# Kernel optimization log

Hardware: AMD Instinct MI355X
Metric: run time of the kernel (lower is better)

Reference implementation:

```python
import jax, jax.numpy as jnp
import numpy as np

B, T, D, K = 64, 4096, 90, 32
LOG2PI = 1.8378770664093453


def setup_inputs() -> dict:
    key = jax.random.key(0)
    k1, k2, k3, k4, k5 = jax.random.split(key, 5)
    X = jax.random.normal(k1, (B, T, D), dtype=jnp.float32)
    state_priors = jax.random.uniform(k2, (K,), dtype=jnp.float32)
    transition_matrix = jax.random.uniform(k3, (K, K), dtype=jnp.float32)
    mu = jax.random.normal(k4, (K, D), dtype=jnp.float32) * 0.5
    log_var = jax.random.normal(k5, (K, D), dtype=jnp.float32) * 0.1
    return {"X": X, "state_priors": state_priors,
            "transition_matrix": transition_matrix, "mu": mu, "log_var": log_var}


def _emission_logprobs(X, mu, log_var):
    # Diagonal-Gaussian log density per state: (B,T,K)
    # expand (x-mu)^2*inv_var to avoid materializing a (B,T,K,D) tensor
    inv_var = jnp.exp(-log_var)                                   # (K,D)
    quad = (jnp.einsum('btd,kd->btk', X * X, inv_var)
            - 2.0 * jnp.einsum('btd,kd->btk', X, mu * inv_var)
            + jnp.sum(mu * mu * inv_var, axis=-1))                # (B,T,K)
    return -0.5 * (quad + jnp.sum(log_var, axis=-1) + D * LOG2PI)


def reference(X, state_priors, transition_matrix, mu, log_var):
    log_A = jax.nn.log_softmax(transition_matrix, axis=1)   # (K,K)
    log_pi = jax.nn.log_softmax(state_priors, axis=0)       # (K,)
    em = _emission_logprobs(X, mu, log_var)                 # (B,T,K)

    log_alpha0 = log_pi + em[:, 0, :]                       # (B,K)

    def step(log_alpha, e_t):
        # log_alpha: (B,K), e_t: (B,K)
        la = e_t + jax.nn.logsumexp(log_alpha[:, :, None] + log_A[None], axis=1)
        return la, None

    em_rest = jnp.swapaxes(em[:, 1:, :], 0, 1)              # (T-1,B,K)
    log_alpha_T, _ = jax.lax.scan(step, log_alpha0, em_rest)
    # sum over subjects of logsumexp over states at final timestep
    return jnp.sum(jax.nn.logsumexp(log_alpha_T, axis=-1))
```

## Files before the change

### kernel.cpp

```cpp
#include <hip/hip_runtime.h>
#include <stdint.h>

#define B_ 64
#define T_ 4096
#define D_ 90
#define K_ 32
#define CH_ 32
#define F_  128
#define NB_ 2048

typedef float f32x16 __attribute__((ext_vector_type(16)));
typedef __bf16 bf16x8 __attribute__((ext_vector_type(8)));

#define WS_A     0
#define WS_PI    1024
#define WS_C0    1056
#define WS_WF    1088
#define WS_EACC  4160
#define WS_MS    12352
#define WS_E0    20544
#define WS_Q2    22080

#define LDS_XOFF(w) ((w) * 768)
#define LDS_WF      3072
#define LDS_TOT     9216

__device__ __forceinline__ int perm_r(int r) {
  int t2 = (r >> 2) & 3;
  return r + ((t2 == 1) ? 4 : (t2 == 2) ? -4 : 0);
}
__device__ __forceinline__ uint32_t pk2(float hi, float lo) {
  return __builtin_amdgcn_perm(__float_as_uint(hi), __float_as_uint(lo), 0x07060302u);
}
__device__ __forceinline__ uint32_t rnd_pk(float hi, float lo) {
  uint32_t uh = __float_as_uint(hi) + 0x8000u;
  uint32_t ul = __float_as_uint(lo) + 0x8000u;
  return __builtin_amdgcn_perm(uh, ul, 0x07060302u);
}
__device__ __forceinline__ float bf2f(ushort u) {
  return __uint_as_float(((uint32_t)u) << 16);
}
__device__ __forceinline__ bf16x8 mkbf(uint32_t a, uint32_t b, uint32_t c, uint32_t d) {
  union { uint32_t u[4]; bf16x8 v; } x;
  x.u[0] = a; x.u[1] = b; x.u[2] = c; x.u[3] = d;
  return x.v;
}

__global__ __launch_bounds__(1024) void prep_kernel(
    const float* __restrict__ priors, const float* __restrict__ trans,
    const float* __restrict__ mu, const float* __restrict__ lv,
    float* __restrict__ ws) {
  int tid = threadIdx.x;
  {
    float v = trans[tid];
    float m = v;
    #pragma unroll
    for (int mk = 16; mk; mk >>= 1) m = fmaxf(m, __shfl_xor(m, mk));
    float e = expf(v - m);
    float s = e;
    #pragma unroll
    for (int mk = 16; mk; mk >>= 1) s += __shfl_xor(s, mk);
    ws[WS_A + tid] = e / s;
  }
  if (tid < 32) {
    float v = priors[tid];
    float m = v;
    #pragma unroll
    for (int mk = 16; mk; mk >>= 1) m = fmaxf(m, __shfl_xor(m, mk));
    float e = expf(v - m);
    float s = e;
    #pragma unroll
    for (int mk = 16; mk; mk >>= 1) s += __shfl_xor(s, mk);
    ws[WS_PI + tid] = e / s;
  }
  for (int i = tid; i < 6144; i += 1024) {
    int j = i & 7, l = (i >> 3) & 63, cm = i >> 9;
    int c = cm >> 1, mat = cm & 1;
    int h = l >> 5, nn = l & 31;
    int d = 16 * c + 8 * h + j;
    float v = 0.0f;
    if (d < D_) {
      float ivd = expf(-lv[nn * D_ + d]);
      v = (mat == 0) ? -0.5f * ivd : mu[nn * D_ + d] * ivd;
    }
    ((ushort*)(ws + WS_WF))[i] = (ushort)((__float_as_uint(v) + 0x8000u) >> 16);
  }
  if (tid < 32) {
    float s = 0.0f;
    for (int d = 0; d < D_; ++d) {
      float l  = lv[tid * D_ + d];
      float iv = expf(-l);
      float m_ = mu[tid * D_ + d];
      s += m_ * m_ * iv + l;
    }
    ws[WS_C0 + tid] = -0.5f * (s + (float)D_ * 1.8378770664093453f);
  }
}

__global__ __launch_bounds__(256, 8) void fused_kernel(const float* __restrict__ X,
                                                       float* __restrict__ ws,
                                                       float* __restrict__ out) {
  __shared__ __align__(16) ushort sh[LDS_TOT];
  __shared__ float msb[4];
  __shared__ int   peb[4];
  int tid = threadIdx.x;
  int l = tid & 63, w = tid >> 6;
  int n = l & 31, h = l >> 5;
  int tB = blockIdx.x << 7;
  int t0 = tB + (w << 5);
  int b  = t0 >> 12;
  if (blockIdx.x == 0 && tid == 0) *out = 0.0f;

  {
    const uint4* wfp = (const uint4*)((const ushort*)(ws + WS_WF));
    uint4* wfl = (uint4*)(sh + LDS_WF);
    #pragma unroll
    for (int k = 0; k < 3; ++k) wfl[tid + (k << 8)] = wfp[tid + (k << 8)];
  }
  float c0 = ws[WS_C0 + n];

  int srow = l >> 1, sp = l & 1;
  const float* xg = X + (size_t)(t0 + srow) * D_ + 8 * sp;
  ushort* xbuf = sh + LDS_XOFF(w);
  float2 va[4];
  auto xload = [&](int c) {
    #pragma unroll
    for (int s = 0; s < 4; ++s) {
      int d = 16 * c + 8 * sp + 2 * s;
      if (d < D_) va[s] = *(const float2*)(xg + 16 * c + 2 * s);
      else { va[s].x = 0.0f; va[s].y = 0.0f; }
    }
  };
  auto xwrite = [&]() {
    uint4 pkv;
    pkv.x = rnd_pk(va[0].y, va[0].x);
    pkv.y = rnd_pk(va[1].y, va[1].x);
    pkv.z = rnd_pk(va[2].y, va[2].x);
    pkv.w = rnd_pk(va[3].y, va[3].x);
    *(uint4*)(xbuf + srow * 24 + 8 * sp) = pkv;
  };
  xload(0);
  xwrite();
  xload(1);
  __syncthreads();

  const ushort* wfl = sh + LDS_WF;
  f32x16 acc;
  #pragma unroll
  for (int r = 0; r < 16; ++r) acc[r] = 0.0f;
  #pragma unroll
  for (int c = 0; c < 6; ++c) {
    union { uint4 u; bf16x8 v; } xb;
    xb.u = *(const uint4*)(xbuf + n * 24 + 8 * h);
    float x[8];
    #pragma unroll
    for (int j = 0; j < 8; ++j) {
      uint32_t uu = ((const uint32_t*)&xb.u)[j >> 1];
      x[j] = bf2f((j & 1) ? (ushort)(uu >> 16) : (ushort)(uu & 0xFFFF));
    }
    union { uint32_t u[4]; bf16x8 v; } x2b;
    #pragma unroll
    for (int r = 0; r < 4; ++r)
      x2b.u[r] = rnd_pk(x[2*r+1] * x[2*r+1], x[2*r] * x[2*r]);
    union { uint4 u; bf16x8 v; } w1, w2;
    w2.u = *(const uint4*)(wfl + (2 * c)     * 512 + l * 8);
    w1.u = *(const uint4*)(wfl + (2 * c + 1) * 512 + l * 8);
    acc = __builtin_amdgcn_mfma_f32_32x32x16_bf16(xb.v,  w1.v, acc, 0, 0, 0);
    acc = __builtin_amdgcn_mfma_f32_32x32x16_bf16(x2b.v, w2.v, acc, 0, 0, 0);
    if (c < 5) {
      xwrite();
      if (c < 4) xload(c + 2);
    }
  }
  float em[16], mrow[16];
  #pragma unroll
  for (int r = 0; r < 16; ++r) {
    float v = acc[r] + c0;
    em[r] = v;
    float m = v;
    #pragma unroll
    for (int mk = 1; mk <= 16; mk <<= 1) m = fmaxf(m, __shfl_xor(m, mk));
    mrow[r] = m;
  }
  uint32_t ebf[8];
  #pragma unroll
  for (int q = 0; q < 4; ++q) {
    float e0 = exp2f((em[4*q]   - mrow[4*q])   * 1.44269504088896f);
    float e1 = exp2f((em[4*q+1] - mrow[4*q+1]) * 1.44269504088896f);
    float e2 = exp2f((em[4*q+2] - mrow[4*q+2]) * 1.44269504088896f);
    float e3 = exp2f((em[4*q+3] - mrow[4*q+3]) * 1.44269504088896f);
    ebf[2*q]     = rnd_pk(e1, e0);
    ebf[2*q + 1] = rnd_pk(e3, e2);
  }
  bool first = ((t0 & (T_ - 1)) == 0);
  if (first && h == 0)
    ((ushort*)(ws + WS_E0))[b * K_ + n] = (ushort)(ebf[0] & 0xFFFF);
  float msum = 0.0f;
  #pragma unroll
  for (int r = 0; r < 16; ++r) msum += mrow[r];
  msum += __shfl_xor(msum, 32);
  if (l == 0) msb[w] = msum;
  __syncthreads();

  int col = perm_r(n);
  const float* A = ws + WS_A;
  float astat[16];
  #pragma unroll
  for (int j = 0; j < 8; ++j) {
    astat[j]     = A[(8 * h + j) * K_ + col];
    astat[8 + j] = A[(16 + 8 * h + j) * K_ + col];
  }
  uint32_t q[8];
  #pragma unroll
  for (int r = 0; r < 4; ++r) {
    int s0 = 8 * h + 2 * r;
    uint32_t lo = (s0 == n)     ? 0x3F80u : 0u;
    uint32_t hi = (s0 + 1 == n) ? 0x3F80u : 0u;
    q[r] = lo | (hi << 16);
    int s2 = s0 + 16;
    lo = (s2 == n)     ? 0x3F80u : 0u;
    hi = (s2 + 1 == n) ? 0x3F80u : 0u;
    q[4 + r] = lo | (hi << 16);
  }
  int eacc = 0;
  const f32x16 z = {0.f,0.f,0.f,0.f,0.f,0.f,0.f,0.f,0.f,0.f,0.f,0.f,0.f,0.f,0.f,0.f};
  #pragma unroll
  for (int r = 0; r < 16; ++r) acc[r] = 0.0f;

  auto step = [&](float e0) {
    uint32_t au[8];
    #pragma unroll
    for (int r = 0; r < 4; ++r) {
      au[r]     = pk2(astat[2 * r + 1] * e0, astat[2 * r] * e0);
      au[4 + r] = pk2(astat[8 + 2 * r + 1] * e0, astat[8 + 2 * r] * e0);
    }
    bf16x8 alo = mkbf(au[0], au[1], au[2], au[3]);
    bf16x8 ahi = mkbf(au[4], au[5], au[6], au[7]);
    bf16x8 qlo = mkbf(q[0], q[1], q[2], q[3]);
    bf16x8 qhi = mkbf(q[4], q[5], q[6], q[7]);
    acc = __builtin_amdgcn_mfma_f32_32x32x16_bf16(alo, qlo, z, 0, 0, 0);
    acc = __builtin_amdgcn_mfma_f32_32x32x16_bf16(ahi, qhi, acc, 0, 0, 0);
    #pragma unroll
    for (int r = 0; r < 4; ++r) {
      q[r]     = pk2(acc[2 * r + 1], acc[2 * r]);
      q[4 + r] = pk2(acc[8 + 2 * r + 1], acc[8 + 2 * r]);
    }
  };
  auto lmul = [&](uint4 lo, uint4 hi) {
    bf16x8 alo = mkbf(lo.x, lo.y, lo.z, lo.w);
    bf16x8 ahi = mkbf(hi.x, hi.y, hi.z, hi.w);
    bf16x8 qlo = mkbf(q[0], q[1], q[2], q[3]);
    bf16x8 qhi = mkbf(q[4], q[5], q[6], q[7]);
    acc = __builtin_amdgcn_mfma_f32_32x32x16_bf16(alo, qlo, z, 0, 0, 0);
    acc = __builtin_amdgcn_mfma_f32_32x32x16_bf16(ahi, qhi, acc, 0, 0, 0);
    #pragma unroll
    for (int r = 0; r < 4; ++r) {
      q[r]     = pk2(acc[2 * r + 1], acc[2 * r]);
      q[4 + r] = pk2(acc[8 + 2 * r + 1], acc[8 + 2 * r]);
    }
  };
  auto renorm = [&]() {
    float m = acc[0];
    #pragma unroll
    for (int r = 1; r < 16; ++r) m = fmaxf(m, acc[r]);
    #pragma unroll
    for (int mk = 1; mk <= 32; mk <<= 1) m = fmaxf(m, __shfl_xor(m, mk));
    int ex;
    frexpf(m, &ex);
    float sc = ldexpf(1.0f, -ex);
    eacc += ex;
    #pragma unroll
    for (int r = 0; r < 16; ++r) acc[r] *= sc;
    #pragma unroll
    for (int r = 0; r < 4; ++r) {
      q[r]     = pk2(acc[2 * r + 1], acc[2 * r]);
      q[4 + r] = pk2(acc[8 + 2 * r + 1], acc[8 + 2 * r]);
    }
  };

  int src0 = col, src1 = col + 32;
  #pragma unroll
  for (int t = 0; t < 32; ++t) {
    uint32_t ed = (uint32_t)__shfl((int)ebf[2 * (t >> 3) + ((t >> 1) & 1)],
                                   ((t >> 2) & 1) ? src1 : src0);
    float e0 = bf2f((t & 1) ? (ushort)(ed >> 16) : (ushort)(ed & 0xFFFF));
    if (t > 0) step(e0);
    else if (!first) step(e0);
    if ((t & 7) == 7) renorm();
  }

  ushort* Qw = sh + w * 1280;
  #pragma unroll
  for (int r = 0; r < 16; ++r) {
    int m_ = (r & 3) + 8 * (r >> 2) + 4 * h;
    Qw[perm_r(m_) * 40 + n] = (ushort)(__float_as_uint(acc[r]) >> 16);
  }
  if (l == 0) peb[w] = eacc;
  __syncthreads();
  if (w != 0) return;

  #pragma unroll
  for (int r = 0; r < 4; ++r) {
    int s0 = 8 * h + 2 * r;
    uint32_t lo = (s0 == n)     ? 0x3F80u : 0u;
    uint32_t hi = (s0 + 1 == n) ? 0x3F80u : 0u;
    q[r] = lo | (hi << 16);
    int s2 = s0 + 16;
    lo = (s2 == n)     ? 0x3F80u : 0u;
    hi = (s2 + 1 == n) ? 0x3F80u : 0u;
    q[4 + r] = lo | (hi << 16);
  }
  eacc = peb[0] + peb[1] + peb[2] + peb[3];
  float msm = msb[0] + msb[1] + msb[2] + msb[3];
  #pragma unroll
  for (int p = 0; p < 4; ++p) {
    const ushort* base = sh + p * 1280 + col * 40;
    uint4 lo = *(const uint4*)(base + 8 * h);
    uint4 hi = *(const uint4*)(base + 16 + 8 * h);
    lmul(lo, hi);
  }
  renorm();
  ushort* Qo = (ushort*)(ws + WS_Q2) + (size_t)blockIdx.x * (K_ * K_);
  #pragma unroll
  for (int r = 0; r < 16; ++r) {
    int m_ = (r & 3) + 8 * (r >> 2) + 4 * h;
    Qo[perm_r(m_) * K_ + n] = (ushort)(__float_as_uint(acc[r]) >> 16);
  }
  if (l == 0) {
    ((int*)ws)[WS_EACC + blockIdx.x] = eacc;
    ws[WS_MS + blockIdx.x] = msm;
  }
}

__global__ __launch_bounds__(256) void combine_kernel(float* __restrict__ ws,
                                                      float* __restrict__ out) {
  __shared__ __align__(16) ushort pm[4][1280];
  __shared__ int pe[4];
  int tid = threadIdx.x;
  int l = tid & 63, w = tid >> 6;
  int h = l >> 5, n = l & 31;
  int b = blockIdx.x;
  int row = perm_r(n);
  int eacc;
  {
    const int* ea = ((const int*)ws) + WS_EACC + b * 32 + w * 8;
    int v = (l < 8) ? ea[l] : 0;
    #pragma unroll
    for (int mk = 1; mk <= 4; mk <<= 1) v += __shfl_xor(v, mk);
    eacc = __shfl(v, 0);
  }
  uint32_t q[8];
  #pragma unroll
  for (int r = 0; r < 4; ++r) {
    int s0 = 8 * h + 2 * r;
    uint32_t lo = (s0 == n)     ? 0x3F80u : 0u;
    uint32_t hi = (s0 + 1 == n) ? 0x3F80u : 0u;
    q[r] = lo | (hi << 16);
    int s2 = s0 + 16;
    lo = (s2 == n)     ? 0x3F80u : 0u;
    hi = (s2 + 1 == n) ? 0x3F80u : 0u;
    q[4 + r] = lo | (hi << 16);
  }
  f32x16 acc;
  #pragma unroll
  for (int r = 0; r < 16; ++r) acc[r] = 0.0f;
  const f32x16 z = {0.f,0.f,0.f,0.f,0.f,0.f,0.f,0.f,0.f,0.f,0.f,0.f,0.f,0.f,0.f,0.f};

  auto lmul = [&](uint4 lo, uint4 hi) {
    bf16x8 alo = mkbf(lo.x, lo.y, lo.z, lo.w);
    bf16x8 ahi = mkbf(hi.x, hi.y, hi.z, hi.w);
    bf16x8 qlo = mkbf(q[0], q[1], q[2], q[3]);
    bf16x8 qhi = mkbf(q[4], q[5], q[6], q[7]);
    acc = __builtin_amdgcn_mfma_f32_32x32x16_bf16(alo, qlo, z, 0, 0, 0);
    acc = __builtin_amdgcn_mfma_f32_32x32x16_bf16(ahi, qhi, acc, 0, 0, 0);
    #pragma unroll
    for (int r = 0; r < 4; ++r) {
      q[r]     = pk2(acc[2 * r + 1], acc[2 * r]);
      q[4 + r] = pk2(acc[8 + 2 * r + 1], acc[8 + 2 * r]);
    }
  };
  auto renorm = [&]() {
    float m = acc[0];
    #pragma unroll
    for (int r = 1; r < 16; ++r) m = fmaxf(m, acc[r]);
    #pragma unroll
    for (int mk = 1; mk <= 32; mk <<= 1) m = fmaxf(m, __shfl_xor(m, mk));
    int ex;
    frexpf(m, &ex);
    float sc = ldexpf(1.0f, -ex);
    eacc += ex;
    #pragma unroll
    for (int r = 0; r < 16; ++r) acc[r] *= sc;
    #pragma unroll
    for (int r = 0; r < 4; ++r) {
      q[r]     = pk2(acc[2 * r + 1], acc[2 * r]);
      q[4 + r] = pk2(acc[8 + 2 * r + 1], acc[8 + 2 * r]);
    }
  };

  const ushort* Qb = (const ushort*)(ws + WS_Q2) + (size_t)(b * 32 + w * 8) * (K_ * K_);
  #pragma unroll
  for (int p = 0; p < 8; ++p) {
    const ushort* Mc = Qb + (size_t)p * (K_ * K_) + row * K_;
    uint4 lo = *(const uint4*)(Mc + 8 * h);
    uint4 hi = *(const uint4*)(Mc + 16 + 8 * h);
    lmul(lo, hi);
    if ((p & 3) == 3) renorm();
  }
  #pragma unroll
  for (int r = 0; r < 16; ++r) {
    int m_ = (r & 3) + 8 * (r >> 2) + 4 * h;
    pm[w][perm_r(m_) * 40 + n] = (ushort)(__float_as_uint(acc[r]) >> 16);
  }
  if (l == 0) pe[w] = eacc;
  __syncthreads();
  if (w != 0) return;

  float alpha0 = ws[WS_PI + n] * bf2f(((const ushort*)(ws + WS_E0))[b * K_ + n]);
  float msm;
  {
    float v = (l < 32) ? ws[WS_MS + b * 32 + l] : 0.0f;
    #pragma unroll
    for (int mk = 1; mk <= 32; mk <<= 1) v += __shfl_xor(v, mk);
    msm = v;
  }
  #pragma unroll
  for (int r = 0; r < 4; ++r) {
    int s0 = 8 * h + 2 * r;
    uint32_t lo = (s0 == n)     ? 0x3F80u : 0u;
    uint32_t hi = (s0 + 1 == n) ? 0x3F80u : 0u;
    q[r] = lo | (hi << 16);
    int s2 = s0 + 16;
    lo = (s2 == n)     ? 0x3F80u : 0u;
    hi = (s2 + 1 == n) ? 0x3F80u : 0u;
    q[4 + r] = lo | (hi << 16);
  }
  #pragma unroll
  for (int r = 0; r < 16; ++r) acc[r] = 0.0f;
  int et = pe[0] + pe[1] + pe[2] + pe[3];
  #pragma unroll
  for (int p = 0; p < 4; ++p) {
    const ushort* base = pm[p] + row * 40;
    uint4 lo = *(const uint4*)(base + 8 * h);
    uint4 hi = *(const uint4*)(base + 16 + 8 * h);
    lmul(lo, hi);
  }
  float part = 0.0f;
  #pragma unroll
  for (int r = 0; r < 16; ++r) part += acc[r];
  part *= alpha0;
  #pragma unroll
  for (int mk = 1; mk <= 32; mk <<= 1) part += __shfl_xor(part, mk);
  if (l == 0) {
    float res = logf(part) + (float)et * 0.69314718055994531f + msm;
    atomicAdd(out, res);
  }
}

extern "C" void kernel_launch(void* const* d_in, const int* in_sizes, int n_in,
                              void* d_out, int out_size, void* d_ws, size_t ws_size,
                              hipStream_t stream) {
  (void)in_sizes; (void)n_in; (void)out_size; (void)ws_size;
  const float* X      = (const float*)d_in[0];
  const float* priors = (const float*)d_in[1];
  const float* trans  = (const float*)d_in[2];
  const float* mu     = (const float*)d_in[3];
  const float* lv     = (const float*)d_in[4];
  float* ws  = (float*)d_ws;
  float* out = (float*)d_out;
  prep_kernel<<<1, 1024, 0, stream>>>(priors, trans, mu, lv, ws);
  fused_kernel<<<NB_, 256, 0, stream>>>(X, ws, out);
  combine_kernel<<<B_, 256, 0, stream>>>(ws, out);
}
```

Before: 197.4 us.

## Stage emission probabilities through per-wave LDS instead of cross-lane shuffles

Each wave now writes its bf16 exponentiated emissions into its own LDS region and reads them back as 8-element vectors, replacing the per-step __shfl lane exchange in the sequential recurrence loop. A block-wide __syncthreads between emission and recurrence is dropped since each wave only reads its own region, and the first-chunk skip is handled by peeling the first group. The LDS footprint grows, so the occupancy hint is lowered from 8 to 6 blocks per SM. The t-loop is no longer fully unrolled, which may cost some scheduling freedom.

```diff
diff --git a/kernel.cpp b/kernel.cpp
--- a/kernel.cpp
+++ b/kernel.cpp
@@ -21,9 +21,9 @@
 #define WS_E0    20544
 #define WS_Q2    22080
 
-#define LDS_XOFF(w) ((w) * 768)
-#define LDS_WF      3072
-#define LDS_TOT     9216
+#define LDS_WREG(w) ((w) * 1280)
+#define LDS_WF      5120
+#define LDS_TOT     11264
 
 __device__ __forceinline__ int perm_r(int r) {
   int t2 = (r >> 2) & 3;
@@ -97,7 +97,7 @@
   }
 }
 
-__global__ __launch_bounds__(256, 8) void fused_kernel(const float* __restrict__ X,
+__global__ __launch_bounds__(256, 6) void fused_kernel(const float* __restrict__ X,
                                                        float* __restrict__ ws,
                                                        float* __restrict__ out) {
   __shared__ __align__(16) ushort sh[LDS_TOT];
@@ -121,7 +121,7 @@
 
   int srow = l >> 1, sp = l & 1;
   const float* xg = X + (size_t)(t0 + srow) * D_ + 8 * sp;
-  ushort* xbuf = sh + LDS_XOFF(w);
+  ushort* xbuf = sh + LDS_WREG(w);
   float2 va[4];
   auto xload = [&](int c) {
     #pragma unroll
@@ -182,25 +182,25 @@
     for (int mk = 1; mk <= 16; mk <<= 1) m = fmaxf(m, __shfl_xor(m, mk));
     mrow[r] = m;
   }
-  uint32_t ebf[8];
+  ushort* Ew = sh + LDS_WREG(w);
   #pragma unroll
   for (int q = 0; q < 4; ++q) {
     float e0 = exp2f((em[4*q]   - mrow[4*q])   * 1.44269504088896f);
     float e1 = exp2f((em[4*q+1] - mrow[4*q+1]) * 1.44269504088896f);
     float e2 = exp2f((em[4*q+2] - mrow[4*q+2]) * 1.44269504088896f);
     float e3 = exp2f((em[4*q+3] - mrow[4*q+3]) * 1.44269504088896f);
-    ebf[2*q]     = rnd_pk(e1, e0);
-    ebf[2*q + 1] = rnd_pk(e3, e2);
-  }
-  bool first = ((t0 & (T_ - 1)) == 0);
-  if (first && h == 0)
-    ((ushort*)(ws + WS_E0))[b * K_ + n] = (ushort)(ebf[0] & 0xFFFF);
+    uint2 d;
+    d.x = rnd_pk(e1, e0);
+    d.y = rnd_pk(e3, e2);
+    *(uint2*)(Ew + n * 40 + 8 * q + 4 * h) = d;
+    if (q == 0 && h == 0 && (t0 & (T_ - 1)) == 0)
+      ((ushort*)(ws + WS_E0))[b * K_ + n] = (ushort)(d.x & 0xFFFF);
+  }
   float msum = 0.0f;
   #pragma unroll
   for (int r = 0; r < 16; ++r) msum += mrow[r];
   msum += __shfl_xor(msum, 32);
   if (l == 0) msb[w] = msum;
-  __syncthreads();
 
   int col = perm_r(n);
   const float* A = ws + WS_A;
@@ -278,18 +278,29 @@
     }
   };
 
-  int src0 = col, src1 = col + 32;
-  #pragma unroll
-  for (int t = 0; t < 32; ++t) {
-    uint32_t ed = (uint32_t)__shfl((int)ebf[2 * (t >> 3) + ((t >> 1) & 1)],
-                                   ((t >> 2) & 1) ? src1 : src0);
-    float e0 = bf2f((t & 1) ? (ushort)(ed >> 16) : (ushort)(ed & 0xFFFF));
-    if (t > 0) step(e0);
-    else if (!first) step(e0);
-    if ((t & 7) == 7) renorm();
-  }
-
-  ushort* Qw = sh + w * 1280;
+  const ushort* Eb = sh + LDS_WREG(w) + col * 40;
+  int g0 = 0;
+  if ((t0 & (T_ - 1)) == 0) {
+    uint4 ev = *(const uint4*)(Eb);
+    #pragma unroll
+    for (int j = 1; j < 8; ++j) {
+      uint32_t u = ((const uint32_t*)&ev)[j >> 1];
+      step(bf2f((j & 1) ? (ushort)(u >> 16) : (ushort)(u & 0xFFFF)));
+    }
+    renorm();
+    g0 = 1;
+  }
+  for (int g = g0; g < CH_ / 8; ++g) {
+    uint4 ev = *(const uint4*)(Eb + 8 * g);
+    #pragma unroll
+    for (int j = 0; j < 8; ++j) {
+      uint32_t u = ((const uint32_t*)&ev)[j >> 1];
+      step(bf2f((j & 1) ? (ushort)(u >> 16) : (ushort)(u & 0xFFFF)));
+    }
+    renorm();
+  }
+
+  ushort* Qw = sh + LDS_WREG(w);
   #pragma unroll
   for (int r = 0; r < 16; ++r) {
     int m_ = (r & 3) + 8 * (r >> 2) + 4 * h;
@@ -314,7 +325,7 @@
   float msm = msb[0] + msb[1] + msb[2] + msb[3];
   #pragma unroll
   for (int p = 0; p < 4; ++p) {
-    const ushort* base = sh + p * 1280 + col * 40;
+    const ushort* base = sh + LDS_WREG(p) + col * 40;
     uint4 lo = *(const uint4*)(base + 8 * h);
     uint4 hi = *(const uint4*)(base + 16 + 8 * h);
     lmul(lo, hi);
```

After: 174.6 us. -11.6%, faster.
